# Performance work log

Measured on AMD Instinct MI355X. Metric: run time of the kernel, lower is better.

## Reference

```python
import jax, jax.numpy as jnp
import numpy as np

K = 7          # local window
STRIDE = 1
PAD = 3
M = 8          # channel groups
C = 256
CQ = C // M    # key/query channels (32)
MID = int(0.5 * CQ)  # geometry prior hidden (16)
B, H, W = 4, 56, 56


def _unfold(x, k, stride, pad):
    """torch.nn.Unfold equivalent -> (B, C, L, k, k) with L = ho*wo."""
    b, c, h, w = x.shape
    xp = jnp.pad(x, ((0, 0), (0, 0), (pad, pad), (pad, pad)))
    ho = (h + 2 * pad - k) // stride + 1
    wo = (w + 2 * pad - k) // stride + 1
    cols = jnp.stack(
        [xp[:, :, i:i + stride * ho:stride, j:j + stride * wo:stride]
         for i in range(k) for j in range(k)], axis=-1)  # (B,C,ho,wo,k*k)
    return cols.reshape(b, c, ho * wo, k, k), ho, wo


def _geometry_position(k):
    a = jnp.arange(-(k // 2), k // 2 + 1, dtype=jnp.float32)
    x_pos = jnp.broadcast_to(a[None, :], (k, k))
    b_r = jnp.arange(k // 2, -(k // 2) - 1, -1, dtype=jnp.float32)
    y_pos = jnp.broadcast_to(b_r[:, None], (k, k))
    return jnp.stack([x_pos, y_pos], axis=0)  # (2, k, k)


def setup_inputs() -> dict:
    key = jax.random.key(0)
    ks = jax.random.split(key, 12)
    s = 0.05
    return {
        "x": jax.random.normal(ks[0], (B, C, H, W), jnp.float32),
        "w_k": jax.random.normal(ks[1], (CQ, C), jnp.float32) * s,
        "b_k": jax.random.normal(ks[2], (CQ,), jnp.float32) * s,
        "w_q": jax.random.normal(ks[3], (CQ, C), jnp.float32) * s,
        "b_q": jax.random.normal(ks[4], (CQ,), jnp.float32) * s,
        "w_g1": jax.random.normal(ks[5], (MID, 2), jnp.float32) * s,
        "b_g1": jax.random.normal(ks[6], (MID,), jnp.float32) * s,
        "w_g2": jax.random.normal(ks[7], (CQ, MID), jnp.float32) * s,
        "b_g2": jax.random.normal(ks[8], (CQ,), jnp.float32) * s,
        "w_f": jax.random.normal(ks[9], (C, C), jnp.float32) * s,
        "b_f": jax.random.normal(ks[10], (C,), jnp.float32) * s,
    }


def reference(x, w_k, b_k, w_q, b_q, w_g1, b_g1, w_g2, b_g2, w_f, b_f):
    b = x.shape[0]
    # key/query maps: 1x1 convs C -> CQ
    km = jnp.einsum('bchw,oc->bohw', x, w_k) + b_k[None, :, None, None]
    qm = jnp.einsum('bchw,oc->bohw', x, w_q) + b_q[None, :, None, None]

    km_u, ho, wo = _unfold(km, K, STRIDE, PAD)   # (B,CQ,L,k,k)
    qm_u, _, _ = _unfold(qm, K, STRIDE, PAD)
    center = K * K // 2
    q_center = qm_u.reshape(b, CQ, ho * wo, K * K)[:, :, :, center]  # (B,CQ,L)
    ak = km_u * q_center[:, :, :, None, None]    # (B,CQ,L,k,k)

    # geometry prior: two 1x1 convs on (2,k,k) position grid
    pos = _geometry_position(K)                                   # (2,k,k)
    g1 = jax.nn.relu(jnp.einsum('pij,op->oij', pos, w_g1) + b_g1[:, None, None])
    gpk = jnp.einsum('pij,op->oij', g1, w_g2) + b_g2[:, None, None]  # (CQ,k,k)

    # NOTE: softmax over the LAST k dim only (faithful to original dim=-1)
    ck = jax.nn.softmax(ak + gpk[None, :, None, :, :], axis=-1)   # (B,CQ,L,k,k)

    x_u, _, _ = _unfold(x, K, STRIDE, PAD)                        # (B,C,L,k,k)
    x_u = x_u.reshape(b, M, CQ, ho * wo, K, K)
    # ck broadcasts across the m groups
    pre = jnp.einsum('bclij,bgclij->bgcl', ck, x_u)               # (B,M,CQ,L)
    pre = pre.reshape(b, C, ho, wo)

    out = jnp.einsum('bchw,oc->bohw', pre, w_f) + b_f[None, :, None, None]
    return out
```

## Files before the change

### kernel.cpp

```cpp
#include <hip/hip_runtime.h>
#include <hip/hip_bf16.h>

typedef __hip_bfloat16 bf16;
typedef __attribute__((ext_vector_type(8))) short short8;
typedef __attribute__((ext_vector_type(4))) float floatx4;

#define B_   4
#define C_   256
#define CQ_  32
#define M_   8
#define MID_ 16
#define H_   56
#define W_   56
#define HW_  3136
#define K_   7

__device__ __forceinline__ unsigned short f2bf(float f) {
    __hip_bfloat16 h = __float2bfloat16(f);
    return *(unsigned short*)&h;
}

__global__ void setup_kernel(const float* __restrict__ wk, const float* __restrict__ wq,
                             const float* __restrict__ wf,
                             const float* __restrict__ wg1, const float* __restrict__ bg1,
                             const float* __restrict__ wg2, const float* __restrict__ bg2,
                             bf16* __restrict__ wkqb, bf16* __restrict__ wfp,
                             float* __restrict__ gpk) {
    int bid = blockIdx.x, t = threadIdx.x;
    if (bid < 64) {
        int i = bid * 256 + t;
        wkqb[i] = __float2bfloat16(i < 8192 ? wk[i] : wq[i - 8192]);
    } else if (bid < 320) {
        int j  = (bid - 64) * 256 + t;
        int ch = j >> 8, kk = j & 255;
        int cq = kk >> 3, m = kk & 7;
        wfp[j] = __float2bfloat16(wf[ch * 256 + m * 32 + cq]);
    } else {
        int idx = (bid - 320) * 256 + t;
        if (idx >= CQ_ * 49) return;
        int cq = idx / 49, ij = idx % 49;
        int i = ij / 7, j = ij % 7;
        float xp = (float)(j - 3);
        float yp = (float)(3 - i);
        float acc = bg2[cq];
        #pragma unroll
        for (int o = 0; o < MID_; o++) {
            float g1 = wg1[o * 2 + 0] * xp + wg1[o * 2 + 1] * yp + bg1[o];
            acc += wg2[cq * MID_ + o] * fmaxf(g1, 0.0f);
        }
        gpk[idx] = acc;
    }
}

__global__ void __launch_bounds__(256) kq_mfma(const float* __restrict__ x,
                                               const bf16* __restrict__ wkqb,
                                               const float* __restrict__ b_k,
                                               const float* __restrict__ b_q,
                                               float* __restrict__ km, float* __restrict__ qm) {
    __shared__ short lt[32 * 264];
    int hw0 = blockIdx.x * 32;
    int b   = blockIdx.y;
    int t   = threadIdx.x;

    {
        int pq = t & 7, cb = t >> 3;
        const float* xb = x + (size_t)b * C_ * HW_ + hw0 + pq * 4;
        #pragma unroll
        for (int ii = 0; ii < 4; ii++) {
            int c = ii * 64 + cb * 2;
            floatx4 fa = *(const floatx4*)(xb + (size_t)c * HW_);
            floatx4 fb = *(const floatx4*)(xb + (size_t)(c + 1) * HW_);
            int c8 = c >> 3, sub = c & 7;
            #pragma unroll
            for (int u = 0; u < 4; u++) {
                int px = pq * 4 + u;
                unsigned uu = (unsigned)f2bf(fa[u]) | ((unsigned)f2bf(fb[u]) << 16);
                int off = px * 264 + ((c8 + (px >> 2)) & 31) * 8 + sub;
                *(unsigned*)&lt[off] = uu;
            }
        }
    }
    __syncthreads();

    int wave = t >> 6, lane = t & 63, quad = lane >> 4, nl = lane & 15;
    int m0 = wave * 16;
    const short* arow = (const short*)wkqb + (m0 + nl) * C_ + quad * 8;
    short8 af[8];
    #pragma unroll
    for (int k0 = 0; k0 < 8; k0++) af[k0] = *(const short8*)(arow + k0 * 32);

    floatx4 acc[2];
    #pragma unroll
    for (int nt = 0; nt < 2; nt++) acc[nt] = (floatx4){0.f, 0.f, 0.f, 0.f};

    #pragma unroll
    for (int nt = 0; nt < 2; nt++) {
        int px = nt * 16 + nl;
        int prow = px * 264, sw = px >> 2;
        #pragma unroll
        for (int k0 = 0; k0 < 8; k0++) {
            int c8 = k0 * 4 + quad;
            short8 bf = *(const short8*)&lt[prow + ((c8 + sw) & 31) * 8];
            acc[nt] = __builtin_amdgcn_mfma_f32_16x16x32_bf16(af[k0], bf, acc[nt], 0, 0, 0);
        }
    }

    #pragma unroll
    for (int r = 0; r < 4; r++) {
        int ch = m0 + quad * 4 + r;
        bool isK = (ch < 32);
        int c = isK ? ch : ch - 32;
        float bias = isK ? b_k[c] : b_q[c];
        float* dst = (isK ? km : qm) + ((size_t)b * CQ_ + c) * HW_ + hw0 + nl;
        dst[0]  = acc[0][r] + bias;
        dst[16] = acc[1][r] + bias;
    }
}

__global__ void __launch_bounds__(448) core_kernel(const float* __restrict__ x,
                                                   const float* __restrict__ km,
                                                   const float* __restrict__ qm,
                                                   const float* __restrict__ gpk,
                                                   bf16* __restrict__ pret) {
    __shared__ float   kms[14 * 62];
    __shared__ floatx4 xs4[2][14 * 62];

    int ht = blockIdx.x, cq = blockIdx.y, b = blockIdx.z;
    int h0 = ht * 8, t = threadIdx.x;

    const float* kmc = km + ((size_t)b * CQ_ + cq) * HW_;
    for (int idx = t; idx < 868; idx += 448) {
        int rr = idx / 62, cc = idx % 62;
        int gh = h0 + rr - 3, gw = cc - 3;
        bool in = ((unsigned)gh < 56u) && ((unsigned)gw < 56u);
        int o = gh * 56 + gw;
        kms[idx] = in ? kmc[o] : 0.f;
        #pragma unroll
        for (int g = 0; g < 2; g++) {
            floatx4 v;
            #pragma unroll
            for (int mm = 0; mm < 4; mm++) {
                const float* xc = x + ((size_t)b * C_ + (g * 4 + mm) * CQ_ + cq) * HW_;
                v[mm] = in ? xc[o] : 0.f;
            }
            xs4[g][idx] = v;
        }
    }
    __syncthreads();

    int r = t / 56, w = t % 56, h = h0 + r;
    float q = qm[((size_t)b * CQ_ + cq) * HW_ + h * 56 + w];
    const float* gp = gpk + cq * 49;

    float ck[49];
    #pragma unroll
    for (int i = 0; i < 7; i++) {
        int base = (r + i) * 62 + w;
        float v[7], s = 0.f;
        #pragma unroll
        for (int j = 0; j < 7; j++) {
            v[j] = __expf(kms[base + j] * q + gp[i * 7 + j]);
            s += v[j];
        }
        float inv = 1.0f / s;
        #pragma unroll
        for (int j = 0; j < 7; j++) ck[i * 7 + j] = v[j] * inv;
    }

    floatx4 a0 = {0.f, 0.f, 0.f, 0.f}, a1 = {0.f, 0.f, 0.f, 0.f};
    #pragma unroll
    for (int i = 0; i < 7; i++) {
        int base = (r + i) * 62 + w;
        #pragma unroll
        for (int j = 0; j < 7; j++) {
            float c = ck[i * 7 + j];
            a0 += c * xs4[0][base + j];
            a1 += c * xs4[1][base + j];
        }
    }

    short8 o8;
    #pragma unroll
    for (int mm = 0; mm < 4; mm++) {
        o8[mm]     = (short)f2bf(a0[mm]);
        o8[mm + 4] = (short)f2bf(a1[mm]);
    }
    *(short8*)((short*)pret + ((size_t)b * HW_ + h * 56 + w) * C_ + cq * 8) = o8;
}

__global__ void __launch_bounds__(256) fconv_mfma(const bf16* __restrict__ pret,
                                                  const bf16* __restrict__ wfp,
                                                  const float* __restrict__ b_f,
                                                  float* __restrict__ out) {
    int hw0 = blockIdx.x * 64;
    int bm  = blockIdx.y;
    int b   = blockIdx.z;
    int t   = threadIdx.x, wave = t >> 6, lane = t & 63, quad = lane >> 4, nl = lane & 15;
    int m0  = bm * 64 + wave * 16;

    const short* arow = (const short*)wfp + (m0 + nl) * C_ + quad * 8;
    short8 af[8];
    #pragma unroll
    for (int k0 = 0; k0 < 8; k0++) af[k0] = *(const short8*)(arow + k0 * 32);

    floatx4 acc[4];
    #pragma unroll
    for (int nt = 0; nt < 4; nt++) acc[nt] = (floatx4){0.f, 0.f, 0.f, 0.f};

    const short* pb = (const short*)pret + ((size_t)b * HW_ + hw0 + nl) * C_ + quad * 8;
    #pragma unroll
    for (int nt = 0; nt < 4; nt++) {
        const short* bp = pb + (size_t)nt * 16 * C_;
        #pragma unroll
        for (int k0 = 0; k0 < 8; k0++)
            acc[nt] = __builtin_amdgcn_mfma_f32_16x16x32_bf16(af[k0], *(const short8*)(bp + k0 * 32),
                                                              acc[nt], 0, 0, 0);
    }

    #pragma unroll
    for (int r = 0; r < 4; r++) {
        int ch = m0 + quad * 4 + r;
        float bias = b_f[ch];
        float* dst = out + ((size_t)b * C_ + ch) * HW_ + hw0 + nl;
        #pragma unroll
        for (int nt = 0; nt < 4; nt++)
            dst[nt * 16] = acc[nt][r] + bias;
    }
}

extern "C" void kernel_launch(void* const* d_in, const int* in_sizes, int n_in,
                              void* d_out, int out_size, void* d_ws, size_t ws_size,
                              hipStream_t stream) {
    const float* x    = (const float*)d_in[0];
    const float* w_k  = (const float*)d_in[1];
    const float* b_k  = (const float*)d_in[2];
    const float* w_q  = (const float*)d_in[3];
    const float* b_q  = (const float*)d_in[4];
    const float* w_g1 = (const float*)d_in[5];
    const float* b_g1 = (const float*)d_in[6];
    const float* w_g2 = (const float*)d_in[7];
    const float* b_g2 = (const float*)d_in[8];
    const float* w_f  = (const float*)d_in[9];
    const float* b_f  = (const float*)d_in[10];
    float* out = (float*)d_out;

    float* ws   = (float*)d_ws;
    float* km   = ws;
    float* qm   = km + (size_t)B_ * CQ_ * HW_;
    float* gpk  = qm + (size_t)B_ * CQ_ * HW_;
    bf16*  wkqb = (bf16*)(gpk + CQ_ * 49);
    bf16*  wfp  = wkqb + 64 * C_;
    bf16*  pret = wfp + C_ * C_;

    setup_kernel<<<dim3(327), 256, 0, stream>>>(w_k, w_q, w_f, w_g1, b_g1, w_g2, b_g2,
                                                wkqb, wfp, gpk);
    kq_mfma<<<dim3(HW_ / 32, B_), 256, 0, stream>>>(x, wkqb, b_k, b_q, km, qm);
    core_kernel<<<dim3(7, CQ_, B_), 448, 0, stream>>>(x, km, qm, gpk, pret);
    fconv_mfma<<<dim3(HW_ / 64, C_ / 64, B_), 256, 0, stream>>>(pret, wfp, b_f, out);
}
```

Before: 126.9 us.

## Fuse local attention with output 1x1 conv and merge setup into key/query kernel

Cuts the pipeline from four kernels to two. Weight conversion and the geometry prior now run inside the key/query MFMA kernel, and the per-pixel windowed softmax-aggregate is fused with the final 256x256 1x1 conv through LDS, so the bf16 pre-activation tensor is never written to or read back from global memory. The key, query and geometry maps are also stored in bf16 to halve their traffic. In exchange the fused kernel launches only 224 blocks of one image row each, keeps 64 float accumulators per thread, reloads x eight times in a serial loop behind barriers, and applies more bf16 rounding to the softmax inputs.

```diff
diff --git a/kernel.cpp b/kernel.cpp
--- a/kernel.cpp
+++ b/kernel.cpp
@@ -8,60 +8,54 @@
 #define B_   4
 #define C_   256
 #define CQ_  32
-#define M_   8
 #define MID_ 16
-#define H_   56
-#define W_   56
 #define HW_  3136
-#define K_   7
 
 __device__ __forceinline__ unsigned short f2bf(float f) {
     __hip_bfloat16 h = __float2bfloat16(f);
     return *(unsigned short*)&h;
 }
-
-__global__ void setup_kernel(const float* __restrict__ wk, const float* __restrict__ wq,
-                             const float* __restrict__ wf,
-                             const float* __restrict__ wg1, const float* __restrict__ bg1,
-                             const float* __restrict__ wg2, const float* __restrict__ bg2,
-                             bf16* __restrict__ wkqb, bf16* __restrict__ wfp,
-                             float* __restrict__ gpk) {
+__device__ __forceinline__ float bf2f(short s) {
+    return __uint_as_float(((unsigned)(unsigned short)s) << 16);
+}
+
+__global__ void __launch_bounds__(256) k1_kernel(const float* __restrict__ x,
+        const float* __restrict__ w_k, const float* __restrict__ b_k,
+        const float* __restrict__ w_q, const float* __restrict__ b_q,
+        const float* __restrict__ w_f,
+        const float* __restrict__ wg1, const float* __restrict__ bg1,
+        const float* __restrict__ wg2, const float* __restrict__ bg2,
+        short* __restrict__ km, short* __restrict__ qm,
+        short* __restrict__ wfp, short* __restrict__ gpkb) {
     int bid = blockIdx.x, t = threadIdx.x;
-    if (bid < 64) {
-        int i = bid * 256 + t;
-        wkqb[i] = __float2bfloat16(i < 8192 ? wk[i] : wq[i - 8192]);
-    } else if (bid < 320) {
-        int j  = (bid - 64) * 256 + t;
-        int ch = j >> 8, kk = j & 255;
-        int cq = kk >> 3, m = kk & 7;
-        wfp[j] = __float2bfloat16(wf[ch * 256 + m * 32 + cq]);
-    } else {
-        int idx = (bid - 320) * 256 + t;
-        if (idx >= CQ_ * 49) return;
-        int cq = idx / 49, ij = idx % 49;
-        int i = ij / 7, j = ij % 7;
-        float xp = (float)(j - 3);
-        float yp = (float)(3 - i);
-        float acc = bg2[cq];
-        #pragma unroll
-        for (int o = 0; o < MID_; o++) {
-            float g1 = wg1[o * 2 + 0] * xp + wg1[o * 2 + 1] * yp + bg1[o];
-            acc += wg2[cq * MID_ + o] * fmaxf(g1, 0.0f);
-        }
-        gpk[idx] = acc;
-    }
-}
-
-__global__ void __launch_bounds__(256) kq_mfma(const float* __restrict__ x,
-                                               const bf16* __restrict__ wkqb,
-                                               const float* __restrict__ b_k,
-                                               const float* __restrict__ b_q,
-                                               float* __restrict__ km, float* __restrict__ qm) {
+    if (bid >= 392) {
+        if (bid < 408) {
+            int base = (bid - 392) * 4096;
+            #pragma unroll
+            for (int s = 0; s < 16; s++) {
+                int j = base + s * 256 + t;
+                int ch = j >> 8, kk = j & 255;
+                wfp[j] = (short)f2bf(w_f[ch * 256 + (kk & 7) * 32 + (kk >> 3)]);
+            }
+        } else {
+            for (int idx = t; idx < CQ_ * 49; idx += 256) {
+                int cq = idx / 49, ij = idx % 49;
+                int i = ij / 7, j = ij % 7;
+                float xp = (float)(j - 3), yp = (float)(3 - i);
+                float acc = bg2[cq];
+                #pragma unroll
+                for (int o = 0; o < MID_; o++) {
+                    float g1 = wg1[o * 2] * xp + wg1[o * 2 + 1] * yp + bg1[o];
+                    acc += wg2[cq * MID_ + o] * fmaxf(g1, 0.f);
+                }
+                gpkb[idx] = (short)f2bf(acc);
+            }
+        }
+        return;
+    }
     __shared__ short lt[32 * 264];
-    int hw0 = blockIdx.x * 32;
-    int b   = blockIdx.y;
-    int t   = threadIdx.x;
-
+    int hw0 = (bid % 98) * 32;
+    int b   = bid / 98;
     {
         int pq = t & 7, cb = t >> 3;
         const float* xb = x + (size_t)b * C_ * HW_ + hw0 + pq * 4;
@@ -75,8 +69,7 @@
             for (int u = 0; u < 4; u++) {
                 int px = pq * 4 + u;
                 unsigned uu = (unsigned)f2bf(fa[u]) | ((unsigned)f2bf(fb[u]) << 16);
-                int off = px * 264 + ((c8 + (px >> 2)) & 31) * 8 + sub;
-                *(unsigned*)&lt[off] = uu;
+                *(unsigned*)&lt[px * 264 + ((c8 + (px >> 2)) & 31) * 8 + sub] = uu;
             }
         }
     }
@@ -84,24 +77,30 @@
 
     int wave = t >> 6, lane = t & 63, quad = lane >> 4, nl = lane & 15;
     int m0 = wave * 16;
-    const short* arow = (const short*)wkqb + (m0 + nl) * C_ + quad * 8;
+    int row = m0 + nl;
+    const float* wsrc = (row < 32) ? (w_k + row * C_) : (w_q + (row - 32) * C_);
+
     short8 af[8];
     #pragma unroll
-    for (int k0 = 0; k0 < 8; k0++) af[k0] = *(const short8*)(arow + k0 * 32);
-
-    floatx4 acc[2];
-    #pragma unroll
-    for (int nt = 0; nt < 2; nt++) acc[nt] = (floatx4){0.f, 0.f, 0.f, 0.f};
-
+    for (int k0 = 0; k0 < 8; k0++) {
+        floatx4 fa = *(const floatx4*)(wsrc + quad * 8 + k0 * 32);
+        floatx4 fb = *(const floatx4*)(wsrc + quad * 8 + k0 * 32 + 4);
+        short8 v;
+        #pragma unroll
+        for (int u = 0; u < 4; u++) { v[u] = (short)f2bf(fa[u]); v[u + 4] = (short)f2bf(fb[u]); }
+        af[k0] = v;
+    }
+
+    floatx4 acc0 = {0.f,0.f,0.f,0.f}, acc1 = {0.f,0.f,0.f,0.f};
     #pragma unroll
     for (int nt = 0; nt < 2; nt++) {
         int px = nt * 16 + nl;
         int prow = px * 264, sw = px >> 2;
         #pragma unroll
         for (int k0 = 0; k0 < 8; k0++) {
-            int c8 = k0 * 4 + quad;
-            short8 bf = *(const short8*)&lt[prow + ((c8 + sw) & 31) * 8];
-            acc[nt] = __builtin_amdgcn_mfma_f32_16x16x32_bf16(af[k0], bf, acc[nt], 0, 0, 0);
+            short8 bf = *(const short8*)&lt[prow + (((k0 * 4 + quad) + sw) & 31) * 8];
+            if (nt == 0) acc0 = __builtin_amdgcn_mfma_f32_16x16x32_bf16(af[k0], bf, acc0, 0, 0, 0);
+            else         acc1 = __builtin_amdgcn_mfma_f32_16x16x32_bf16(af[k0], bf, acc1, 0, 0, 0);
         }
     }
 
@@ -111,120 +110,134 @@
         bool isK = (ch < 32);
         int c = isK ? ch : ch - 32;
         float bias = isK ? b_k[c] : b_q[c];
-        float* dst = (isK ? km : qm) + ((size_t)b * CQ_ + c) * HW_ + hw0 + nl;
-        dst[0]  = acc[0][r] + bias;
-        dst[16] = acc[1][r] + bias;
-    }
-}
-
-__global__ void __launch_bounds__(448) core_kernel(const float* __restrict__ x,
-                                                   const float* __restrict__ km,
-                                                   const float* __restrict__ qm,
-                                                   const float* __restrict__ gpk,
-                                                   bf16* __restrict__ pret) {
-    __shared__ float   kms[14 * 62];
-    __shared__ floatx4 xs4[2][14 * 62];
-
-    int ht = blockIdx.x, cq = blockIdx.y, b = blockIdx.z;
-    int h0 = ht * 8, t = threadIdx.x;
-
-    const float* kmc = km + ((size_t)b * CQ_ + cq) * HW_;
-    for (int idx = t; idx < 868; idx += 448) {
-        int rr = idx / 62, cc = idx % 62;
-        int gh = h0 + rr - 3, gw = cc - 3;
-        bool in = ((unsigned)gh < 56u) && ((unsigned)gw < 56u);
-        int o = gh * 56 + gw;
-        kms[idx] = in ? kmc[o] : 0.f;
-        #pragma unroll
-        for (int g = 0; g < 2; g++) {
-            floatx4 v;
-            #pragma unroll
-            for (int mm = 0; mm < 4; mm++) {
-                const float* xc = x + ((size_t)b * C_ + (g * 4 + mm) * CQ_ + cq) * HW_;
-                v[mm] = in ? xc[o] : 0.f;
-            }
-            xs4[g][idx] = v;
-        }
-    }
-    __syncthreads();
-
-    int r = t / 56, w = t % 56, h = h0 + r;
-    float q = qm[((size_t)b * CQ_ + cq) * HW_ + h * 56 + w];
-    const float* gp = gpk + cq * 49;
-
-    float ck[49];
-    #pragma unroll
-    for (int i = 0; i < 7; i++) {
-        int base = (r + i) * 62 + w;
-        float v[7], s = 0.f;
-        #pragma unroll
-        for (int j = 0; j < 7; j++) {
-            v[j] = __expf(kms[base + j] * q + gp[i * 7 + j]);
-            s += v[j];
-        }
-        float inv = 1.0f / s;
-        #pragma unroll
-        for (int j = 0; j < 7; j++) ck[i * 7 + j] = v[j] * inv;
-    }
-
-    floatx4 a0 = {0.f, 0.f, 0.f, 0.f}, a1 = {0.f, 0.f, 0.f, 0.f};
-    #pragma unroll
-    for (int i = 0; i < 7; i++) {
-        int base = (r + i) * 62 + w;
-        #pragma unroll
-        for (int j = 0; j < 7; j++) {
-            float c = ck[i * 7 + j];
-            a0 += c * xs4[0][base + j];
-            a1 += c * xs4[1][base + j];
-        }
-    }
-
-    short8 o8;
-    #pragma unroll
-    for (int mm = 0; mm < 4; mm++) {
-        o8[mm]     = (short)f2bf(a0[mm]);
-        o8[mm + 4] = (short)f2bf(a1[mm]);
-    }
-    *(short8*)((short*)pret + ((size_t)b * HW_ + h * 56 + w) * C_ + cq * 8) = o8;
-}
-
-__global__ void __launch_bounds__(256) fconv_mfma(const bf16* __restrict__ pret,
-                                                  const bf16* __restrict__ wfp,
-                                                  const float* __restrict__ b_f,
-                                                  float* __restrict__ out) {
-    int hw0 = blockIdx.x * 64;
-    int bm  = blockIdx.y;
-    int b   = blockIdx.z;
-    int t   = threadIdx.x, wave = t >> 6, lane = t & 63, quad = lane >> 4, nl = lane & 15;
-    int m0  = bm * 64 + wave * 16;
-
-    const short* arow = (const short*)wfp + (m0 + nl) * C_ + quad * 8;
-    short8 af[8];
-    #pragma unroll
-    for (int k0 = 0; k0 < 8; k0++) af[k0] = *(const short8*)(arow + k0 * 32);
-
-    floatx4 acc[4];
-    #pragma unroll
-    for (int nt = 0; nt < 4; nt++) acc[nt] = (floatx4){0.f, 0.f, 0.f, 0.f};
-
-    const short* pb = (const short*)pret + ((size_t)b * HW_ + hw0 + nl) * C_ + quad * 8;
-    #pragma unroll
-    for (int nt = 0; nt < 4; nt++) {
-        const short* bp = pb + (size_t)nt * 16 * C_;
-        #pragma unroll
-        for (int k0 = 0; k0 < 8; k0++)
-            acc[nt] = __builtin_amdgcn_mfma_f32_16x16x32_bf16(af[k0], *(const short8*)(bp + k0 * 32),
-                                                              acc[nt], 0, 0, 0);
-    }
-
-    #pragma unroll
-    for (int r = 0; r < 4; r++) {
-        int ch = m0 + quad * 4 + r;
-        float bias = b_f[ch];
-        float* dst = out + ((size_t)b * C_ + ch) * HW_ + hw0 + nl;
-        #pragma unroll
-        for (int nt = 0; nt < 4; nt++)
-            dst[nt * 16] = acc[nt][r] + bias;
+        short* dst = (isK ? km : qm) + ((size_t)b * CQ_ + c) * HW_ + hw0 + nl;
+        dst[0]  = (short)f2bf(acc0[r] + bias);
+        dst[16] = (short)f2bf(acc1[r] + bias);
+    }
+}
+
+__global__ void __launch_bounds__(256) k2_fused(const float* __restrict__ x,
+        const short* __restrict__ km, const short* __restrict__ qm,
+        const short* __restrict__ gpkb, const short* __restrict__ wfp,
+        const float* __restrict__ b_f, float* __restrict__ out) {
+    __shared__ short lds[29856];
+    short* kms  = lds;
+    short* xs   = lds + 14336;
+    short* gpks = lds + 14336 + 13952;
+    short* pre  = lds;
+
+    int h = blockIdx.x, b = blockIdx.y, t = threadIdx.x;
+
+    for (int i = t; i < 1568; i += 256) gpks[i] = gpkb[i];
+    const short* kmg = km + (size_t)b * CQ_ * HW_;
+    for (int u = t; u < 32 * 434; u += 256) {
+        int cq = u / 434, px = u % 434;
+        int i = px / 62, cc = px % 62;
+        int gh = h + i - 3, gw = cc - 3;
+        short v = 0;
+        if ((unsigned)gh < 56u && (unsigned)gw < 56u) v = kmg[cq * HW_ + gh * 56 + gw];
+        kms[cq * 448 + px] = v;
+    }
+    __syncthreads();
+
+    int cqq = t / 56, w = t % 56;
+    bool active = (t < 224);
+    float preacc[8][8];
+    #pragma unroll
+    for (int it = 0; it < 8; it++)
+        #pragma unroll
+        for (int m = 0; m < 8; m++) preacc[it][m] = 0.f;
+
+    #pragma unroll
+    for (int iter = 0; iter < 8; iter++) {
+        __syncthreads();
+        for (int u = t; u < 3472; u += 256) {
+            int px = u % 434, rest = u / 434;
+            int cqi = rest >> 1, mg = rest & 1;
+            int cq = iter * 4 + cqi;
+            int i = px / 62, cc = px % 62;
+            int gh = h + i - 3, gw = cc - 3;
+            unsigned lo = 0, hi = 0;
+            if ((unsigned)gh < 56u && (unsigned)gw < 56u) {
+                const float* xb = x + ((size_t)b * C_ + (mg * 4) * 32 + cq) * HW_ + gh * 56 + gw;
+                lo = (unsigned)f2bf(xb[0])              | ((unsigned)f2bf(xb[32 * HW_]) << 16);
+                hi = (unsigned)f2bf(xb[(size_t)64*HW_]) | ((unsigned)f2bf(xb[(size_t)96*HW_]) << 16);
+            }
+            unsigned long long pk = (unsigned long long)lo | ((unsigned long long)hi << 32);
+            *(unsigned long long*)&xs[(cqi * 436 + px) * 8 + mg * 4] = pk;
+        }
+        __syncthreads();
+        if (active) {
+            int cq = iter * 4 + cqq;
+            float q = bf2f(qm[((size_t)b * CQ_ + cq) * HW_ + h * 56 + w]);
+            const short* kr = kms + cq * 448;
+            const short* gr = gpks + cq * 49;
+            const short* xr = xs + cqq * 436 * 8;
+            #pragma unroll
+            for (int i = 0; i < 7; i++) {
+                float v[7], s = 0.f;
+                int base = i * 62 + w;
+                #pragma unroll
+                for (int j = 0; j < 7; j++) {
+                    v[j] = __expf(bf2f(kr[base + j]) * q + bf2f(gr[i * 7 + j]));
+                    s += v[j];
+                }
+                float inv = 1.0f / s;
+                #pragma unroll
+                for (int j = 0; j < 7; j++) {
+                    float c = v[j] * inv;
+                    short8 xv = *(const short8*)&xr[(base + j) * 8];
+                    #pragma unroll
+                    for (int m = 0; m < 8; m++)
+                        preacc[iter][m] += c * bf2f(xv[m]);
+                }
+            }
+        }
+    }
+    __syncthreads();
+    if (active) {
+        #pragma unroll
+        for (int iter = 0; iter < 8; iter++) {
+            int cq = iter * 4 + cqq;
+            short8 o;
+            #pragma unroll
+            for (int m = 0; m < 8; m++) o[m] = (short)f2bf(preacc[iter][m]);
+            *(short8*)&pre[w * 264 + cq * 8] = o;
+        }
+    }
+    for (int u = t; u < 8 * 264; u += 256) pre[56 * 264 + u] = 0;
+    __syncthreads();
+
+    int wave = t >> 6, lane = t & 63, quad = lane >> 4, nl = lane & 15;
+    #pragma unroll
+    for (int mt = 0; mt < 4; mt++) {
+        int m0 = wave * 64 + mt * 16;
+        const short* arow = wfp + (m0 + nl) * C_ + quad * 8;
+        short8 af[8];
+        #pragma unroll
+        for (int k0 = 0; k0 < 8; k0++) af[k0] = *(const short8*)(arow + k0 * 32);
+        floatx4 acc[4];
+        #pragma unroll
+        for (int nt = 0; nt < 4; nt++) acc[nt] = (floatx4){0.f,0.f,0.f,0.f};
+        #pragma unroll
+        for (int k0 = 0; k0 < 8; k0++) {
+            #pragma unroll
+            for (int nt = 0; nt < 4; nt++) {
+                short8 bf = *(const short8*)&pre[(nt * 16 + nl) * 264 + k0 * 32 + quad * 8];
+                acc[nt] = __builtin_amdgcn_mfma_f32_16x16x32_bf16(af[k0], bf, acc[nt], 0, 0, 0);
+            }
+        }
+        #pragma unroll
+        for (int r = 0; r < 4; r++) {
+            int ch = m0 + quad * 4 + r;
+            float bias = b_f[ch];
+            float* dst = out + ((size_t)b * C_ + ch) * HW_ + h * 56;
+            #pragma unroll
+            for (int nt = 0; nt < 4; nt++) {
+                int col = nt * 16 + nl;
+                if (col < 56) dst[col] = acc[nt][r] + bias;
+            }
+        }
     }
 }
 
@@ -244,17 +257,13 @@
     const float* b_f  = (const float*)d_in[10];
     float* out = (float*)d_out;
 
-    float* ws   = (float*)d_ws;
-    float* km   = ws;
-    float* qm   = km + (size_t)B_ * CQ_ * HW_;
-    float* gpk  = qm + (size_t)B_ * CQ_ * HW_;
-    bf16*  wkqb = (bf16*)(gpk + CQ_ * 49);
-    bf16*  wfp  = wkqb + 64 * C_;
-    bf16*  pret = wfp + C_ * C_;
-
-    setup_kernel<<<dim3(327), 256, 0, stream>>>(w_k, w_q, w_f, w_g1, b_g1, w_g2, b_g2,
-                                                wkqb, wfp, gpk);
-    kq_mfma<<<dim3(HW_ / 32, B_), 256, 0, stream>>>(x, wkqb, b_k, b_q, km, qm);
-    core_kernel<<<dim3(7, CQ_, B_), 448, 0, stream>>>(x, km, qm, gpk, pret);
-    fconv_mfma<<<dim3(HW_ / 64, C_ / 64, B_), 256, 0, stream>>>(pret, wfp, b_f, out);
-}
+    short* ws   = (short*)d_ws;
+    short* km   = ws;
+    short* qm   = km + (size_t)B_ * CQ_ * HW_;
+    short* wfp  = qm + (size_t)B_ * CQ_ * HW_;
+    short* gpkb = wfp + C_ * C_;
+
+    k1_kernel<<<dim3(409), 256, 0, stream>>>(x, w_k, b_k, w_q, b_q, w_f,
+                                             w_g1, b_g1, w_g2, b_g2, km, qm, wfp, gpkb);
+    k2_fused<<<dim3(56, B_), 256, 0, stream>>>(x, km, qm, gpkb, wfp, b_f, out);
+}
```

Result: slower. 212.0 us (+67.1%).

## Fuse setup into kq kernel and pack core tile as bf16 with folded softmax

Applied to the files above, without the earlier changes.

Merges the weight-setup kernel into the key/query projection kernel, which now converts w_k/w_q to bf16 inline and uses extra blocks for the w_f permute and geometry prior. This removes one launch and a round trip through global memory. The core kernel stages x in shared memory as packed bf16 with vectorized float4 loads and explicit halo zeroing. Softmax normalization is applied per row after accumulation instead of storing 49 weights, which lowers register pressure and LDS footprint but adds bf16 rounding of x before the weighted sum.

```diff
diff --git a/kernel.cpp b/kernel.cpp
--- a/kernel.cpp
+++ b/kernel.cpp
@@ -8,103 +8,103 @@
 #define B_   4
 #define C_   256
 #define CQ_  32
-#define M_   8
 #define MID_ 16
-#define H_   56
-#define W_   56
 #define HW_  3136
-#define K_   7
 
 __device__ __forceinline__ unsigned short f2bf(float f) {
     __hip_bfloat16 h = __float2bfloat16(f);
     return *(unsigned short*)&h;
 }
-
-__global__ void setup_kernel(const float* __restrict__ wk, const float* __restrict__ wq,
-                             const float* __restrict__ wf,
-                             const float* __restrict__ wg1, const float* __restrict__ bg1,
-                             const float* __restrict__ wg2, const float* __restrict__ bg2,
-                             bf16* __restrict__ wkqb, bf16* __restrict__ wfp,
-                             float* __restrict__ gpk) {
+__device__ __forceinline__ float bf2f(short s) {
+    return __uint_as_float(((unsigned)(unsigned short)s) << 16);
+}
+
+__global__ void __launch_bounds__(256) kq_setup(const float* __restrict__ x,
+        const float* __restrict__ w_k, const float* __restrict__ b_k,
+        const float* __restrict__ w_q, const float* __restrict__ b_q,
+        const float* __restrict__ w_f,
+        const float* __restrict__ wg1, const float* __restrict__ bg1,
+        const float* __restrict__ wg2, const float* __restrict__ bg2,
+        float* __restrict__ km, float* __restrict__ qm,
+        short* __restrict__ wfp, float* __restrict__ gpk) {
     int bid = blockIdx.x, t = threadIdx.x;
-    if (bid < 64) {
-        int i = bid * 256 + t;
-        wkqb[i] = __float2bfloat16(i < 8192 ? wk[i] : wq[i - 8192]);
-    } else if (bid < 320) {
-        int j  = (bid - 64) * 256 + t;
-        int ch = j >> 8, kk = j & 255;
-        int cq = kk >> 3, m = kk & 7;
-        wfp[j] = __float2bfloat16(wf[ch * 256 + m * 32 + cq]);
-    } else {
-        int idx = (bid - 320) * 256 + t;
-        if (idx >= CQ_ * 49) return;
-        int cq = idx / 49, ij = idx % 49;
-        int i = ij / 7, j = ij % 7;
-        float xp = (float)(j - 3);
-        float yp = (float)(3 - i);
-        float acc = bg2[cq];
-        #pragma unroll
-        for (int o = 0; o < MID_; o++) {
-            float g1 = wg1[o * 2 + 0] * xp + wg1[o * 2 + 1] * yp + bg1[o];
-            acc += wg2[cq * MID_ + o] * fmaxf(g1, 0.0f);
-        }
-        gpk[idx] = acc;
-    }
-}
-
-__global__ void __launch_bounds__(256) kq_mfma(const float* __restrict__ x,
-                                               const bf16* __restrict__ wkqb,
-                                               const float* __restrict__ b_k,
-                                               const float* __restrict__ b_q,
-                                               float* __restrict__ km, float* __restrict__ qm) {
+    if (bid >= 392) {
+        if (bid < 408) {
+            int base = (bid - 392) * 4096;
+            #pragma unroll
+            for (int s = 0; s < 16; s++) {
+                int j = base + s * 256 + t;
+                wfp[j] = (short)f2bf(w_f[(j >> 8) * 256 + (j & 7) * 32 + ((j & 255) >> 3)]);
+            }
+        } else {
+            for (int idx = t; idx < CQ_ * 49; idx += 256) {
+                int cq = idx / 49, ij = idx % 49;
+                int i = ij / 7, j = ij % 7;
+                float xp = (float)(j - 3), yp = (float)(3 - i);
+                float acc = bg2[cq];
+                #pragma unroll
+                for (int o = 0; o < MID_; o++) {
+                    float g1 = wg1[o * 2] * xp + wg1[o * 2 + 1] * yp + bg1[o];
+                    acc += wg2[cq * MID_ + o] * fmaxf(g1, 0.f);
+                }
+                gpk[idx] = acc;
+            }
+        }
+        return;
+    }
     __shared__ short lt[32 * 264];
-    int hw0 = blockIdx.x * 32;
-    int b   = blockIdx.y;
-    int t   = threadIdx.x;
-
-    {
-        int pq = t & 7, cb = t >> 3;
-        const float* xb = x + (size_t)b * C_ * HW_ + hw0 + pq * 4;
-        #pragma unroll
-        for (int ii = 0; ii < 4; ii++) {
-            int c = ii * 64 + cb * 2;
-            floatx4 fa = *(const floatx4*)(xb + (size_t)c * HW_);
-            floatx4 fb = *(const floatx4*)(xb + (size_t)(c + 1) * HW_);
-            int c8 = c >> 3, sub = c & 7;
-            #pragma unroll
-            for (int u = 0; u < 4; u++) {
-                int px = pq * 4 + u;
-                unsigned uu = (unsigned)f2bf(fa[u]) | ((unsigned)f2bf(fb[u]) << 16);
-                int off = px * 264 + ((c8 + (px >> 2)) & 31) * 8 + sub;
-                *(unsigned*)&lt[off] = uu;
-            }
-        }
-    }
-    __syncthreads();
+    int hw0 = (bid % 98) * 32;
+    int b   = bid / 98;
+
+    int pq = t & 7, cb = t >> 3;
+    const float* xb = x + (size_t)b * C_ * HW_ + hw0 + pq * 4;
+    floatx4 fa[4], fb[4];
+    #pragma unroll
+    for (int ii = 0; ii < 4; ii++) {
+        int c = ii * 64 + cb * 2;
+        fa[ii] = *(const floatx4*)(xb + (size_t)c * HW_);
+        fb[ii] = *(const floatx4*)(xb + (size_t)(c + 1) * HW_);
+    }
+    #pragma unroll
+    for (int ii = 0; ii < 4; ii++) {
+        int c = ii * 64 + cb * 2;
+        int c8 = c >> 3, sub = c & 7;
+        #pragma unroll
+        for (int u = 0; u < 4; u++) {
+            int px = pq * 4 + u;
+            unsigned uu = (unsigned)f2bf(fa[ii][u]) | ((unsigned)f2bf(fb[ii][u]) << 16);
+            *(unsigned*)&lt[px * 264 + ((c8 + (px >> 2)) & 31) * 8 + sub] = uu;
+        }
+    }
 
     int wave = t >> 6, lane = t & 63, quad = lane >> 4, nl = lane & 15;
     int m0 = wave * 16;
-    const short* arow = (const short*)wkqb + (m0 + nl) * C_ + quad * 8;
+    int row = m0 + nl;
+    const float* wsrc = (row < 32) ? (w_k + row * C_) : (w_q + (row - 32) * C_);
     short8 af[8];
     #pragma unroll
-    for (int k0 = 0; k0 < 8; k0++) af[k0] = *(const short8*)(arow + k0 * 32);
-
-    floatx4 acc[2];
-    #pragma unroll
-    for (int nt = 0; nt < 2; nt++) acc[nt] = (floatx4){0.f, 0.f, 0.f, 0.f};
-
+    for (int k0 = 0; k0 < 8; k0++) {
+        floatx4 wa = *(const floatx4*)(wsrc + k0 * 32 + quad * 8);
+        floatx4 wb = *(const floatx4*)(wsrc + k0 * 32 + quad * 8 + 4);
+        short8 v;
+        #pragma unroll
+        for (int u = 0; u < 4; u++) { v[u] = (short)f2bf(wa[u]); v[u + 4] = (short)f2bf(wb[u]); }
+        af[k0] = v;
+    }
+    __syncthreads();
+
+    floatx4 acc0 = {0.f,0.f,0.f,0.f}, acc1 = {0.f,0.f,0.f,0.f};
     #pragma unroll
     for (int nt = 0; nt < 2; nt++) {
         int px = nt * 16 + nl;
         int prow = px * 264, sw = px >> 2;
         #pragma unroll
         for (int k0 = 0; k0 < 8; k0++) {
-            int c8 = k0 * 4 + quad;
-            short8 bf = *(const short8*)&lt[prow + ((c8 + sw) & 31) * 8];
-            acc[nt] = __builtin_amdgcn_mfma_f32_16x16x32_bf16(af[k0], bf, acc[nt], 0, 0, 0);
-        }
-    }
-
+            short8 bfr = *(const short8*)&lt[prow + (((k0 * 4 + quad) + sw) & 31) * 8];
+            if (nt == 0) acc0 = __builtin_amdgcn_mfma_f32_16x16x32_bf16(af[k0], bfr, acc0, 0, 0, 0);
+            else         acc1 = __builtin_amdgcn_mfma_f32_16x16x32_bf16(af[k0], bfr, acc1, 0, 0, 0);
+        }
+    }
     #pragma unroll
     for (int r = 0; r < 4; r++) {
         int ch = m0 + quad * 4 + r;
@@ -112,84 +112,98 @@
         int c = isK ? ch : ch - 32;
         float bias = isK ? b_k[c] : b_q[c];
         float* dst = (isK ? km : qm) + ((size_t)b * CQ_ + c) * HW_ + hw0 + nl;
-        dst[0]  = acc[0][r] + bias;
-        dst[16] = acc[1][r] + bias;
+        dst[0]  = acc0[r] + bias;
+        dst[16] = acc1[r] + bias;
     }
 }
 
 __global__ void __launch_bounds__(448) core_kernel(const float* __restrict__ x,
-                                                   const float* __restrict__ km,
-                                                   const float* __restrict__ qm,
-                                                   const float* __restrict__ gpk,
-                                                   bf16* __restrict__ pret) {
-    __shared__ float   kms[14 * 62];
-    __shared__ floatx4 xs4[2][14 * 62];
+        const float* __restrict__ km, const float* __restrict__ qm,
+        const float* __restrict__ gpk, short* __restrict__ pret) {
+    __shared__ float kms[14 * 64];
+    __shared__ short xs[14 * 64 * 8];
 
     int ht = blockIdx.x, cq = blockIdx.y, b = blockIdx.z;
     int h0 = ht * 8, t = threadIdx.x;
 
     const float* kmc = km + ((size_t)b * CQ_ + cq) * HW_;
-    for (int idx = t; idx < 868; idx += 448) {
-        int rr = idx / 62, cc = idx % 62;
-        int gh = h0 + rr - 3, gw = cc - 3;
-        bool in = ((unsigned)gh < 56u) && ((unsigned)gw < 56u);
-        int o = gh * 56 + gw;
-        kms[idx] = in ? kmc[o] : 0.f;
-        #pragma unroll
-        for (int g = 0; g < 2; g++) {
-            floatx4 v;
+    if (t < 196) {
+        int rr = t / 14, s = t % 14;
+        int gh = h0 + rr - 3;
+        floatx4 v = {0.f,0.f,0.f,0.f};
+        if ((unsigned)gh < 56u) v = *(const floatx4*)&kmc[gh * 56 + s * 4];
+        *(floatx4*)&kms[rr * 64 + 4 + 4 * s] = v;
+    }
+    if (t < 84) {
+        int rr = t / 6, e = t % 6;
+        kms[rr * 64 + ((e < 3) ? 1 + e : 57 + e)] = 0.f;
+    }
+    if (t < 392) {
+        int rr = t / 28, rem = t % 28, s = rem >> 1, mg = rem & 1;
+        int gh = h0 + rr - 3;
+        bool valid = ((unsigned)gh < 56u);
+        floatx4 f[4];
+        #pragma unroll
+        for (int mm = 0; mm < 4; mm++) {
+            int m = mg * 4 + mm;
+            f[mm] = (floatx4){0.f,0.f,0.f,0.f};
+            if (valid) f[mm] = *(const floatx4*)&x[((size_t)b * C_ + m * CQ_ + cq) * HW_ + gh * 56 + s * 4];
+        }
+        #pragma unroll
+        for (int u = 0; u < 4; u++) {
+            int p = 4 + 4 * s + u;
+            unsigned lo = (unsigned)f2bf(f[0][u]) | ((unsigned)f2bf(f[1][u]) << 16);
+            unsigned hi = (unsigned)f2bf(f[2][u]) | ((unsigned)f2bf(f[3][u]) << 16);
+            unsigned long long pk = (unsigned long long)lo | ((unsigned long long)hi << 32);
+            *(unsigned long long*)&xs[(rr * 64 + p) * 8 + mg * 4] = pk;
+        }
+    }
+    if (t < 168) {
+        int rr = t / 12, rem = t % 12, e = rem >> 1, mg = rem & 1;
+        int p = (e < 3) ? 1 + e : 57 + e;
+        *(unsigned long long*)&xs[(rr * 64 + p) * 8 + mg * 4] = 0ull;
+    }
+    __syncthreads();
+
+    int r = t / 56, w = t % 56;
+    float q = qm[((size_t)b * CQ_ + cq) * HW_ + (h0 + r) * 56 + w];
+    const float* gp = gpk + cq * 49;
+
+    float acc[8];
+    #pragma unroll
+    for (int m = 0; m < 8; m++) acc[m] = 0.f;
+
+    #pragma unroll
+    for (int i = 0; i < 7; i++) {
+        const float* kr = &kms[(r + i) * 64 + w + 1];
+        float v[7], s = 0.f;
+        #pragma unroll
+        for (int j = 0; j < 7; j++) {
+            v[j] = __expf(kr[j] * q + gp[i * 7 + j]);
+            s += v[j];
+        }
+        float rm[8];
+        #pragma unroll
+        for (int m = 0; m < 8; m++) rm[m] = 0.f;
+        #pragma unroll
+        for (int j = 0; j < 7; j++) {
+            short8 xv = *(const short8*)&xs[((r + i) * 64 + w + j + 1) * 8];
             #pragma unroll
-            for (int mm = 0; mm < 4; mm++) {
-                const float* xc = x + ((size_t)b * C_ + (g * 4 + mm) * CQ_ + cq) * HW_;
-                v[mm] = in ? xc[o] : 0.f;
-            }
-            xs4[g][idx] = v;
-        }
-    }
-    __syncthreads();
-
-    int r = t / 56, w = t % 56, h = h0 + r;
-    float q = qm[((size_t)b * CQ_ + cq) * HW_ + h * 56 + w];
-    const float* gp = gpk + cq * 49;
-
-    float ck[49];
-    #pragma unroll
-    for (int i = 0; i < 7; i++) {
-        int base = (r + i) * 62 + w;
-        float v[7], s = 0.f;
-        #pragma unroll
-        for (int j = 0; j < 7; j++) {
-            v[j] = __expf(kms[base + j] * q + gp[i * 7 + j]);
-            s += v[j];
+            for (int m = 0; m < 8; m++) rm[m] += v[j] * bf2f(xv[m]);
         }
         float inv = 1.0f / s;
         #pragma unroll
-        for (int j = 0; j < 7; j++) ck[i * 7 + j] = v[j] * inv;
-    }
-
-    floatx4 a0 = {0.f, 0.f, 0.f, 0.f}, a1 = {0.f, 0.f, 0.f, 0.f};
-    #pragma unroll
-    for (int i = 0; i < 7; i++) {
-        int base = (r + i) * 62 + w;
-        #pragma unroll
-        for (int j = 0; j < 7; j++) {
-            float c = ck[i * 7 + j];
-            a0 += c * xs4[0][base + j];
-            a1 += c * xs4[1][base + j];
-        }
+        for (int m = 0; m < 8; m++) acc[m] += inv * rm[m];
     }
 
     short8 o8;
     #pragma unroll
-    for (int mm = 0; mm < 4; mm++) {
-        o8[mm]     = (short)f2bf(a0[mm]);
-        o8[mm + 4] = (short)f2bf(a1[mm]);
-    }
-    *(short8*)((short*)pret + ((size_t)b * HW_ + h * 56 + w) * C_ + cq * 8) = o8;
-}
-
-__global__ void __launch_bounds__(256) fconv_mfma(const bf16* __restrict__ pret,
-                                                  const bf16* __restrict__ wfp,
+    for (int m = 0; m < 8; m++) o8[m] = (short)f2bf(acc[m]);
+    *(short8*)&pret[((size_t)b * HW_ + (h0 + r) * 56 + w) * C_ + cq * 8] = o8;
+}
+
+__global__ void __launch_bounds__(256) fconv_mfma(const short* __restrict__ pret,
+                                                  const short* __restrict__ wfp,
                                                   const float* __restrict__ b_f,
                                                   float* __restrict__ out) {
     int hw0 = blockIdx.x * 64;
@@ -198,16 +212,16 @@
     int t   = threadIdx.x, wave = t >> 6, lane = t & 63, quad = lane >> 4, nl = lane & 15;
     int m0  = bm * 64 + wave * 16;
 
-    const short* arow = (const short*)wfp + (m0 + nl) * C_ + quad * 8;
+    const short* arow = wfp + (m0 + nl) * C_ + quad * 8;
     short8 af[8];
     #pragma unroll
     for (int k0 = 0; k0 < 8; k0++) af[k0] = *(const short8*)(arow + k0 * 32);
 
     floatx4 acc[4];
     #pragma unroll
-    for (int nt = 0; nt < 4; nt++) acc[nt] = (floatx4){0.f, 0.f, 0.f, 0.f};
-
-    const short* pb = (const short*)pret + ((size_t)b * HW_ + hw0 + nl) * C_ + quad * 8;
+    for (int nt = 0; nt < 4; nt++) acc[nt] = (floatx4){0.f,0.f,0.f,0.f};
+
+    const short* pb = pret + ((size_t)b * HW_ + hw0 + nl) * C_ + quad * 8;
     #pragma unroll
     for (int nt = 0; nt < 4; nt++) {
         const short* bp = pb + (size_t)nt * 16 * C_;
@@ -248,13 +262,11 @@
     float* km   = ws;
     float* qm   = km + (size_t)B_ * CQ_ * HW_;
     float* gpk  = qm + (size_t)B_ * CQ_ * HW_;
-    bf16*  wkqb = (bf16*)(gpk + CQ_ * 49);
-    bf16*  wfp  = wkqb + 64 * C_;
-    bf16*  pret = wfp + C_ * C_;
-
-    setup_kernel<<<dim3(327), 256, 0, stream>>>(w_k, w_q, w_f, w_g1, b_g1, w_g2, b_g2,
-                                                wkqb, wfp, gpk);
-    kq_mfma<<<dim3(HW_ / 32, B_), 256, 0, stream>>>(x, wkqb, b_k, b_q, km, qm);
+    short* wfp  = (short*)(gpk + CQ_ * 49);
+    short* pret = wfp + C_ * C_;
+
+    kq_setup<<<dim3(409), 256, 0, stream>>>(x, w_k, b_k, w_q, b_q, w_f,
+                                            w_g1, b_g1, w_g2, b_g2, km, qm, wfp, gpk);
     core_kernel<<<dim3(7, CQ_, B_), 448, 0, stream>>>(x, km, qm, gpk, pret);
     fconv_mfma<<<dim3(HW_ / 64, C_ / 64, B_), 256, 0, stream>>>(pret, wfp, b_f, out);
 }
```

New measurement: 148.0 us. 1.17x slower.
